# Kernel tuning notes

Hardware: AMD Instinct MI355X
Metric: run time of the kernel (lower is better)

Reference implementation:

```python
import jax, jax.numpy as jnp
import numpy as np

B, C, H, W = 8, 1024, 56, 56
NBINS = 256          # torch.histc(bins=256, min=0, max=1)
T_THRESH = 0.9       # EKLM entropy-ratio threshold
NUM_CLASSES = 30


def setup_inputs() -> dict:
    key = jax.random.key(0)
    k1, k2 = jax.random.split(key)
    x = jax.random.uniform(k1, (B, C, H, W), dtype=jnp.float32)
    w_fc = jax.random.normal(k2, (C, NUM_CLASSES), dtype=jnp.float32) * 0.02
    return {"x": x, "w_fc": w_fc}


def _integral_hist(x):
    """One fused pass replacing the per-region torch.histc calls.
    Returns per-(h,w)-cell histograms [H,W,256] and their 2D inclusive
    prefix sum padded to [H+1,W+1,256] so any rectangle histogram is 4 lookups.
    Matches torch.histc semantics: values outside [0,1] ignored, v==1 -> last bin."""
    valid = (x >= 0.0) & (x <= 1.0)
    q = jnp.clip(jnp.floor(x * NBINS), 0, NBINS - 1).astype(jnp.int32)
    q = jnp.where(valid, q, NBINS)  # out-of-range -> extra bin, dropped below
    hh = jnp.broadcast_to(jnp.arange(H)[None, None, :, None], x.shape)
    ww = jnp.broadcast_to(jnp.arange(W)[None, None, None, :], x.shape)
    cell = jnp.zeros((H, W, NBINS + 1), jnp.float32).at[hh, ww, q].add(1.0)[..., :NBINS]
    integ = jnp.cumsum(jnp.cumsum(cell, axis=0), axis=1)
    integ = jnp.pad(integ, ((1, 0), (1, 0), (0, 0)))  # [H+1, W+1, 256]
    return cell, integ


def _entropy_of_hist(h):
    p = h / jnp.sum(h)
    return -jnp.sum(p * jnp.log2(p + 1e-9))


def _region_entropy(integ, xs, xd, ys, yd):
    # histogram of x[:, :, xs:xd, ys:yd] via integral-histogram lookups
    h = integ[xd, yd] - integ[xs, yd] - integ[xd, ys] + integ[xs, ys]
    return _entropy_of_hist(h)


def eklm(x):
    """Entropy-based Key Localization Method (xs fixed to 0, as in source)."""
    cell, integ = _integral_hist(x)
    # compute_entropy_for_each_y: entropy of each [:, :, 0:1, y:y+1] column cell
    col_hists = cell[0]  # [W, 256]
    p = col_hists / jnp.sum(col_hists, axis=1, keepdims=True)
    ent_y = -jnp.sum(p * jnp.log2(p + 1e-9), axis=1)
    ys0 = jnp.argmax(ent_y).astype(jnp.int32)
    total_ent = _region_entropy(integ, 0, H, 0, W)

    def ent(xd, ys, yd):
        return _region_entropy(integ, 0, xd, ys, yd)

    def cond(state):
        xd, ys, yd, Ts, done = state
        return (Ts < T_THRESH) & (~done)

    def body(state):
        xd, ys, yd, Ts, done = state
        e_cur = ent(xd, ys, yd)
        # greedy priority identical to source: grow xd, else shrink ys, else grow yd
        c1 = (xd + 1 < H) & (ent(xd + 1, ys, yd) > e_cur)
        c2 = (~c1) & (ys - 1 >= 0) & (ent(xd, jnp.maximum(ys - 1, 0), yd) > e_cur)
        c3 = (~c1) & (~c2) & (yd + 1 < W) & (ent(xd, ys, jnp.minimum(yd + 1, W)) > e_cur)
        xd_n = jnp.where(c1, xd + 1, xd)
        ys_n = jnp.where(c2, ys - 1, ys)
        yd_n = jnp.where(c3, yd + 1, yd)
        done_n = ~(c1 | c2 | c3)
        Ts_n = ent(xd_n, ys_n, yd_n) / total_ent
        return (xd_n, ys_n, yd_n, Ts_n, done_n)

    xd0 = jnp.int32(1)
    yd0 = ys0 + jnp.int32(1)
    Ts0 = ent(xd0, ys0, yd0) / total_ent
    xd, ys, yd, _, _ = jax.lax.while_loop(
        cond, body, (xd0, ys0, yd0, Ts0, jnp.bool_(False)))
    return jnp.int32(0), xd, ys, yd


def reference(x, w_fc):
    xs, xd, ys, yd = eklm(x)
    # crop the located key region (mask form for static shapes), mean-pool, classify
    row = jnp.arange(H)
    col = jnp.arange(W)
    mask = ((row[:, None] >= xs) & (row[:, None] < xd)
            & (col[None, :] >= ys) & (col[None, :] < yd)).astype(x.dtype)
    area = jnp.maximum(jnp.sum(mask), 1.0)
    pooled = jnp.einsum('bchw,hw->bc', x, mask) / area  # [B, C]
    return pooled @ w_fc  # [B, NUM_CLASSES]
```

## Files before the change

### kernel.cpp

```cpp
#include <hip/hip_runtime.h>
#include <math.h>

#define BB 8
#define CC 1024
#define HH 56
#define WW 56
#define NB 256
#define NCLS 30
#define BC (BB * CC)
#define PLANE (HH * WW)
#define CELLS (HH * WW)
#define SLICES 16
#define WSPLIT 2
#define WHALF (WW / WSPLIT)
#define PL_PER_SLICE (BC / SLICES)
#define HTHREADS 256
#define VEC4_PER_BLOCK (PL_PER_SLICE * WHALF / 4)
#define HIST_ITERS (VEC4_PER_BLOCK / HTHREADS)

template <int PACK, bool ATOMIC_FLUSH>
__global__ __launch_bounds__(HTHREADS) void hist_kernel(const float* __restrict__ x,
                                                        unsigned* __restrict__ dst) {
    constexpr int WPW = NB / PACK;
    constexpr int PITCH = WPW + 1;
    constexpr int LH_TOT = WHALF * PITCH;
    constexpr int FLUSH_N = WPW * WHALF;
    __shared__ unsigned lh[LH_TOT];

    const int tid = threadIdx.x;
    const int g = blockIdx.x;
    const int whalf = (g >> 3) & 1;
    const int hs = ((g >> 4) << 3) | (g & 7);
    const int h = hs % HH;
    const int slice = hs / HH;

    for (int i = tid; i < LH_TOT; i += HTHREADS) lh[i] = 0u;
    __syncthreads();

    const float* __restrict__ xb =
        x + (size_t)(slice * PL_PER_SLICE) * PLANE + h * WW + whalf * WHALF;

#pragma unroll
    for (int it = 0; it < HIST_ITERS; ++it) {
        const int j = it * HTHREADS + tid;
        const int bcl = j / 7;
        const int wq = j - bcl * 7;
        const float4 v = *(const float4*)(xb + (size_t)bcl * PLANE + wq * 4);
        const float vv[4] = {v.x, v.y, v.z, v.w};
#pragma unroll
        for (int e = 0; e < 4; ++e) {
            const float f = vv[e];
            if (f >= 0.f && f <= 1.f) {
                int bin = (int)(f * 256.f);
                if (bin > 255) bin = 255;
                const int sh = (PACK == 4) ? ((bin & 3) << 3) : ((bin & 1) << 4);
                const int word = (PACK == 4) ? (bin >> 2) : (bin >> 1);
                atomicAdd(&lh[(wq * 4 + e) * PITCH + word], 1u << sh);
            }
        }
    }
    __syncthreads();

    for (int i = tid; i < FLUSH_N; i += HTHREADS) {
        const int word = i / WHALF;
        const int wl = i - word * WHALF;
        const unsigned v = lh[wl * PITCH + word];
        const int cell = h * WW + whalf * WHALF + wl;
        if (ATOMIC_FLUSH) {
            if (v) atomicAdd(&dst[(size_t)word * CELLS + cell], v);
        } else {
            dst[((size_t)word * SLICES + slice) * CELLS + cell] = v;
        }
    }
}

#define CPITCH 57
__global__ __launch_bounds__(256) void cum2d4_kernel(const unsigned* __restrict__ ps,
                                                     unsigned* __restrict__ integ) {
    __shared__ unsigned acc[4][HH * CPITCH];
    const int word = blockIdx.x;
    const unsigned* __restrict__ base = ps + (size_t)word * SLICES * CELLS;

    for (int c = threadIdx.x; c < CELLS; c += 256) {
        unsigned s0 = 0, s1 = 0, s2 = 0, s3 = 0;
#pragma unroll
        for (int sl = 0; sl < SLICES; ++sl) {
            const unsigned v = base[(size_t)sl * CELLS + c];
            s0 += v & 0xffu;
            s1 += (v >> 8) & 0xffu;
            s2 += (v >> 16) & 0xffu;
            s3 += v >> 24;
        }
        const int r = c / WW, w = c - r * WW;
        const int a_idx = r * CPITCH + w;
        acc[0][a_idx] = s0; acc[1][a_idx] = s1;
        acc[2][a_idx] = s2; acc[3][a_idx] = s3;
    }
    __syncthreads();

    if (threadIdx.x < 224) {
        const int a = threadIdx.x / HH, r = threadIdx.x % HH;
        unsigned run = 0;
        const int rb = r * CPITCH;
        for (int w = 0; w < WW; ++w) { run += acc[a][rb + w]; acc[a][rb + w] = run; }
    }
    __syncthreads();
    if (threadIdx.x < 224) {
        const int a = threadIdx.x / WW, cw = threadIdx.x % WW;
        unsigned run = 0;
        for (int hh = 0; hh < HH; ++hh) {
            run += acc[a][hh * CPITCH + cw];
            acc[a][hh * CPITCH + cw] = run;
        }
    }
    __syncthreads();

    for (int i = threadIdx.x; i < 4 * CELLS; i += 256) {
        const int a = i / CELLS, c = i - a * CELLS;
        const int r = c / WW, w = c - r * WW;
        integ[(size_t)(word * 4 + a) * CELLS + c] = acc[a][r * CPITCH + w];
    }
}

__global__ __launch_bounds__(256) void cum2d2_kernel(const unsigned* __restrict__ hp,
                                                     unsigned* __restrict__ integ) {
    __shared__ unsigned acc[CELLS];
    const int bin = blockIdx.x;
    const int word = bin >> 1;
    const int sh = (bin & 1) << 4;
    const unsigned* __restrict__ base = hp + (size_t)word * CELLS;

    for (int c = threadIdx.x; c < CELLS; c += 256)
        acc[c] = (base[c] >> sh) & 0xffffu;
    __syncthreads();
    if (threadIdx.x < HH) {
        unsigned run = 0;
        const int rb = threadIdx.x * WW;
        for (int w = 0; w < WW; ++w) { run += acc[rb + w]; acc[rb + w] = run; }
    }
    __syncthreads();
    if (threadIdx.x < WW) {
        unsigned run = 0;
        for (int hh = 0; hh < HH; ++hh) {
            run += acc[hh * WW + threadIdx.x];
            acc[hh * WW + threadIdx.x] = run;
        }
    }
    __syncthreads();
    unsigned* __restrict__ ob = integ + (size_t)bin * CELLS;
    for (int c = threadIdx.x; c < CELLS; c += 256) ob[c] = acc[c];
}

__device__ __forceinline__ float wave_sum(float v) {
#pragma unroll
    for (int off = 32; off > 0; off >>= 1) v += __shfl_xor(v, off);
    return v;
}

__device__ __forceinline__ float ilook(const unsigned* __restrict__ integ,
                                       int a, int b, int bin) {
    return (a == 0 || b == 0)
               ? 0.f
               : (float)integ[(size_t)bin * CELLS + (a - 1) * WW + (b - 1)];
}

__device__ float region_ent(const unsigned* __restrict__ integ, int lane,
                            int xd, int ys, int yd) {
    float hb[4];
    float hs = 0.f;
#pragma unroll
    for (int k = 0; k < 4; k++) {
        const int bin = lane + 64 * k;
        const float hv = ilook(integ, xd, yd, bin) - ilook(integ, xd, ys, bin);
        hb[k] = hv;
        hs += hv;
    }
    hs = wave_sum(hs);
    float e = 0.f;
#pragma unroll
    for (int k = 0; k < 4; k++) {
        const float p = hb[k] / hs;
        e += p * log2f(p + 1e-9f);
    }
    return -wave_sum(e);
}

__global__ __launch_bounds__(1024) void decide_kernel(const unsigned* __restrict__ integ,
                                                      int* __restrict__ region) {
    __shared__ float ent_s[WW];
    const int tid = threadIdx.x;
    const int lane = tid & 63;
    const int wv = tid >> 6;

    for (int w = wv; w < WW; w += 16) {
        float hb[4], hs = 0.f;
#pragma unroll
        for (int k = 0; k < 4; k++) {
            const int bin = lane + 64 * k;
            const float a = (float)integ[(size_t)bin * CELLS + w];
            const float b = w ? (float)integ[(size_t)bin * CELLS + w - 1] : 0.f;
            hb[k] = a - b;
            hs += hb[k];
        }
        hs = wave_sum(hs);
        float e = 0.f;
#pragma unroll
        for (int k = 0; k < 4; k++) {
            const float p = hb[k] / hs;
            e += p * log2f(p + 1e-9f);
        }
        e = -wave_sum(e);
        if (lane == 0) ent_s[w] = e;
    }
    __syncthreads();
    if (wv != 0) return;

    float best = -3.0e38f;
    int bestw = 0;
    for (int w = 0; w < WW; ++w) {
        const float e = ent_s[w];
        if (e > best) { best = e; bestw = w; }
    }

    const float total_ent = region_ent(integ, lane, HH, 0, WW);

    int xd = 1, ys = bestw, yd = bestw + 1;
    float Ts = region_ent(integ, lane, xd, ys, yd) / total_ent;
    bool done = false;
    int iter = 0;
    while (Ts < 0.9f && !done && iter < 1000) {
        iter++;
        const float e_cur = region_ent(integ, lane, xd, ys, yd);
        const int ysm = (ys - 1 < 0) ? 0 : ys - 1;
        const int ydp = (yd + 1 > WW) ? WW : yd + 1;
        const bool c1 = (xd + 1 < HH) && (region_ent(integ, lane, xd + 1, ys, yd) > e_cur);
        const bool c2 = !c1 && (ys - 1 >= 0) && (region_ent(integ, lane, xd, ysm, yd) > e_cur);
        const bool c3 = !c1 && !c2 && (yd + 1 < WW) && (region_ent(integ, lane, xd, ys, ydp) > e_cur);
        if (c1) xd = xd + 1;
        else if (c2) ys = ys - 1;
        else if (c3) yd = yd + 1;
        done = !(c1 || c2 || c3);
        Ts = region_ent(integ, lane, xd, ys, yd) / total_ent;
    }

    if (lane == 0) {
        region[0] = xd;
        region[1] = ys;
        region[2] = yd;
    }
}

__global__ void pool_kernel(const float* __restrict__ x,
                            const int* __restrict__ region,
                            float* __restrict__ pooled) {
    const int bc = blockIdx.x;
    const int xd = region[0], ys = region[1], yd = region[2];
    const int Wd = yd - ys;
    const int n = xd * Wd;
    const float area = fmaxf((float)n, 1.f);
    const float* plane = x + (size_t)bc * PLANE;
    float s = 0.f;
    for (int j = threadIdx.x; j < n; j += 64) {
        const int r = j / Wd;
        const int cc = ys + (j - r * Wd);
        s += plane[r * WW + cc];
    }
#pragma unroll
    for (int off = 32; off > 0; off >>= 1) s += __shfl_xor(s, off);
    if (threadIdx.x == 0) pooled[bc] = s / area;
}

__global__ __launch_bounds__(256) void fc_kernel(const float* __restrict__ pooled,
                                                 const float* __restrict__ wfc,
                                                 float* __restrict__ out) {
    __shared__ float red[240];
    const int b = blockIdx.x;
    const int t = threadIdx.x;
    if (t < 240) {
        const int chunk = t / NCLS;
        const int n = t - chunk * NCLS;
        const float* pv = pooled + b * CC + chunk * 128;
        const float* wv = wfc + (size_t)(chunk * 128) * NCLS + n;
        float a0 = 0.f, a1 = 0.f, a2 = 0.f, a3 = 0.f;
        for (int c = 0; c < 128; c += 4) {
            a0 += pv[c + 0] * wv[(c + 0) * NCLS];
            a1 += pv[c + 1] * wv[(c + 1) * NCLS];
            a2 += pv[c + 2] * wv[(c + 2) * NCLS];
            a3 += pv[c + 3] * wv[(c + 3) * NCLS];
        }
        red[t] = (a0 + a1) + (a2 + a3);
    }
    __syncthreads();
    if (t < NCLS) {
        float s = 0.f;
#pragma unroll
        for (int ch = 0; ch < 8; ++ch) s += red[ch * NCLS + t];
        out[b * NCLS + t] = s;
    }
}

extern "C" void kernel_launch(void* const* d_in, const int* in_sizes, int n_in,
                              void* d_out, int out_size, void* d_ws, size_t ws_size,
                              hipStream_t stream) {
    const float* x = (const float*)d_in[0];
    const float* wfc = (const float*)d_in[1];
    float* out = (float*)d_out;

    unsigned char* ws = (unsigned char*)d_ws;
    const size_t ps_bytes = (size_t)(NB / 4) * SLICES * CELLS * 4;
    const size_t integ_bytes = (size_t)NB * CELLS * 4;
    const size_t needA = ps_bytes + integ_bytes + 4096 + (size_t)BC * 4;

    if (ws_size >= needA) {
        unsigned* ps = (unsigned*)ws;
        unsigned* integ = (unsigned*)(ws + ps_bytes);
        int* region = (int*)(ws + ps_bytes + integ_bytes);
        float* pooled = (float*)(ws + ps_bytes + integ_bytes + 4096);

        hist_kernel<4, false><<<HH * WSPLIT * SLICES, HTHREADS, 0, stream>>>(x, ps);
        cum2d4_kernel<<<NB / 4, 256, 0, stream>>>(ps, integ);
        decide_kernel<<<1, 1024, 0, stream>>>(integ, region);
        pool_kernel<<<BC, 64, 0, stream>>>(x, region, pooled);
        fc_kernel<<<BB, 256, 0, stream>>>(pooled, wfc, out);
    } else {
        unsigned* hp = (unsigned*)ws;
        const size_t hp_bytes = (size_t)(NB / 2) * CELLS * 4;
        unsigned* integ = (unsigned*)(ws + hp_bytes);
        int* region = (int*)(ws + hp_bytes + integ_bytes);
        float* pooled = (float*)(ws + hp_bytes + integ_bytes + 4096);

        hipMemsetAsync(hp, 0, hp_bytes, stream);
        hist_kernel<2, true><<<HH * WSPLIT * SLICES, HTHREADS, 0, stream>>>(x, hp);
        cum2d2_kernel<<<NB, 256, 0, stream>>>(hp, integ);
        decide_kernel<<<1, 1024, 0, stream>>>(integ, region);
        pool_kernel<<<BC, 64, 0, stream>>>(x, region, pooled);
        fc_kernel<<<BB, 256, 0, stream>>>(pooled, wfc, out);
    }
}
```

Baseline: 194.9 us.

## Fuse cumsum with decide and pool with fc via last-block tickets

Cuts the pipeline from five kernels to three. The 2D prefix-sum kernel and the single-block decide kernel are merged: the last block to finish, detected with an atomic ticket, runs the decision. Pooling and the FC layer are merged the same way, with the last pool block computing all outputs. The histogram kernel resets the tickets, changes its block-to-cell mapping, and the pool blocks grow from 64 to 256 threads. The aim is to remove launch gaps, at the cost of serial tail work on one block and atomics plus fences in every block.

```diff
diff --git a/kernel.cpp b/kernel.cpp
--- a/kernel.cpp
+++ b/kernel.cpp
@@ -17,10 +17,13 @@
 #define HTHREADS 256
 #define VEC4_PER_BLOCK (PL_PER_SLICE * WHALF / 4)
 #define HIST_ITERS (VEC4_PER_BLOCK / HTHREADS)
+#define HGRID (HH * WSPLIT * SLICES)
+#define CPITCH 57
 
 template <int PACK, bool ATOMIC_FLUSH>
 __global__ __launch_bounds__(HTHREADS) void hist_kernel(const float* __restrict__ x,
-                                                        unsigned* __restrict__ dst) {
+                                                        unsigned* __restrict__ dst,
+                                                        unsigned* __restrict__ tickets) {
     constexpr int WPW = NB / PACK;
     constexpr int PITCH = WPW + 1;
     constexpr int LH_TOT = WHALF * PITCH;
@@ -28,9 +31,11 @@
     __shared__ unsigned lh[LH_TOT];
 
     const int tid = threadIdx.x;
-    const int g = blockIdx.x;
-    const int whalf = (g >> 3) & 1;
-    const int hs = ((g >> 4) << 3) | (g & 7);
+    const int bid = blockIdx.x;
+    if (bid == 0 && tid < 2) tickets[tid] = 0u;
+
+    const int whalf = bid & (WSPLIT - 1);
+    const int hs = bid / WSPLIT;
     const int h = hs % HH;
     const int slice = hs / HH;
 
@@ -74,83 +79,6 @@
     }
 }
 
-#define CPITCH 57
-__global__ __launch_bounds__(256) void cum2d4_kernel(const unsigned* __restrict__ ps,
-                                                     unsigned* __restrict__ integ) {
-    __shared__ unsigned acc[4][HH * CPITCH];
-    const int word = blockIdx.x;
-    const unsigned* __restrict__ base = ps + (size_t)word * SLICES * CELLS;
-
-    for (int c = threadIdx.x; c < CELLS; c += 256) {
-        unsigned s0 = 0, s1 = 0, s2 = 0, s3 = 0;
-#pragma unroll
-        for (int sl = 0; sl < SLICES; ++sl) {
-            const unsigned v = base[(size_t)sl * CELLS + c];
-            s0 += v & 0xffu;
-            s1 += (v >> 8) & 0xffu;
-            s2 += (v >> 16) & 0xffu;
-            s3 += v >> 24;
-        }
-        const int r = c / WW, w = c - r * WW;
-        const int a_idx = r * CPITCH + w;
-        acc[0][a_idx] = s0; acc[1][a_idx] = s1;
-        acc[2][a_idx] = s2; acc[3][a_idx] = s3;
-    }
-    __syncthreads();
-
-    if (threadIdx.x < 224) {
-        const int a = threadIdx.x / HH, r = threadIdx.x % HH;
-        unsigned run = 0;
-        const int rb = r * CPITCH;
-        for (int w = 0; w < WW; ++w) { run += acc[a][rb + w]; acc[a][rb + w] = run; }
-    }
-    __syncthreads();
-    if (threadIdx.x < 224) {
-        const int a = threadIdx.x / WW, cw = threadIdx.x % WW;
-        unsigned run = 0;
-        for (int hh = 0; hh < HH; ++hh) {
-            run += acc[a][hh * CPITCH + cw];
-            acc[a][hh * CPITCH + cw] = run;
-        }
-    }
-    __syncthreads();
-
-    for (int i = threadIdx.x; i < 4 * CELLS; i += 256) {
-        const int a = i / CELLS, c = i - a * CELLS;
-        const int r = c / WW, w = c - r * WW;
-        integ[(size_t)(word * 4 + a) * CELLS + c] = acc[a][r * CPITCH + w];
-    }
-}
-
-__global__ __launch_bounds__(256) void cum2d2_kernel(const unsigned* __restrict__ hp,
-                                                     unsigned* __restrict__ integ) {
-    __shared__ unsigned acc[CELLS];
-    const int bin = blockIdx.x;
-    const int word = bin >> 1;
-    const int sh = (bin & 1) << 4;
-    const unsigned* __restrict__ base = hp + (size_t)word * CELLS;
-
-    for (int c = threadIdx.x; c < CELLS; c += 256)
-        acc[c] = (base[c] >> sh) & 0xffffu;
-    __syncthreads();
-    if (threadIdx.x < HH) {
-        unsigned run = 0;
-        const int rb = threadIdx.x * WW;
-        for (int w = 0; w < WW; ++w) { run += acc[rb + w]; acc[rb + w] = run; }
-    }
-    __syncthreads();
-    if (threadIdx.x < WW) {
-        unsigned run = 0;
-        for (int hh = 0; hh < HH; ++hh) {
-            run += acc[hh * WW + threadIdx.x];
-            acc[hh * WW + threadIdx.x] = run;
-        }
-    }
-    __syncthreads();
-    unsigned* __restrict__ ob = integ + (size_t)bin * CELLS;
-    for (int c = threadIdx.x; c < CELLS; c += 256) ob[c] = acc[c];
-}
-
 __device__ __forceinline__ float wave_sum(float v) {
 #pragma unroll
     for (int off = 32; off > 0; off >>= 1) v += __shfl_xor(v, off);
@@ -185,14 +113,14 @@
     return -wave_sum(e);
 }
 
-__global__ __launch_bounds__(1024) void decide_kernel(const unsigned* __restrict__ integ,
-                                                      int* __restrict__ region) {
-    __shared__ float ent_s[WW];
+__device__ void decide_body(const unsigned* __restrict__ integ,
+                            int* __restrict__ region, float* ent_s) {
     const int tid = threadIdx.x;
     const int lane = tid & 63;
     const int wv = tid >> 6;
-
-    for (int w = wv; w < WW; w += 16) {
+    const int nw = blockDim.x >> 6;
+
+    for (int w = wv; w < WW; w += nw) {
         float hb[4], hs = 0.f;
 #pragma unroll
         for (int k = 0; k < 4; k++) {
@@ -250,52 +178,157 @@
     }
 }
 
-__global__ void pool_kernel(const float* __restrict__ x,
-                            const int* __restrict__ region,
-                            float* __restrict__ pooled) {
+__global__ __launch_bounds__(1024) void cum2d4_decide_kernel(
+    const unsigned* __restrict__ ps, unsigned* __restrict__ integ,
+    int* __restrict__ region, unsigned* __restrict__ tickets) {
+    __shared__ unsigned acc[4][HH * CPITCH];
+    __shared__ float ent_s[WW];
+    __shared__ unsigned ticket;
+    const int word = blockIdx.x;
+    const unsigned* __restrict__ base = ps + (size_t)word * SLICES * CELLS;
+
+    for (int c = threadIdx.x; c < CELLS; c += 1024) {
+        unsigned s0 = 0, s1 = 0, s2 = 0, s3 = 0;
+#pragma unroll
+        for (int sl = 0; sl < SLICES; ++sl) {
+            const unsigned v = base[(size_t)sl * CELLS + c];
+            s0 += v & 0xffu;
+            s1 += (v >> 8) & 0xffu;
+            s2 += (v >> 16) & 0xffu;
+            s3 += v >> 24;
+        }
+        const int r = c / WW, w = c - r * WW;
+        const int ai = r * CPITCH + w;
+        acc[0][ai] = s0; acc[1][ai] = s1; acc[2][ai] = s2; acc[3][ai] = s3;
+    }
+    __syncthreads();
+
+    if (threadIdx.x < 224) {
+        const int a = threadIdx.x / HH, r = threadIdx.x % HH;
+        unsigned run = 0;
+        const int rb = r * CPITCH;
+        for (int w = 0; w < WW; ++w) { run += acc[a][rb + w]; acc[a][rb + w] = run; }
+    }
+    __syncthreads();
+    if (threadIdx.x < 224) {
+        const int a = threadIdx.x / WW, cw = threadIdx.x % WW;
+        unsigned run = 0;
+        for (int hh = 0; hh < HH; ++hh) {
+            run += acc[a][hh * CPITCH + cw];
+            acc[a][hh * CPITCH + cw] = run;
+        }
+    }
+    __syncthreads();
+
+    for (int i = threadIdx.x; i < 4 * CELLS; i += 1024) {
+        const int a = i / CELLS, c = i - a * CELLS;
+        const int r = c / WW, w = c - r * WW;
+        integ[(size_t)(word * 4 + a) * CELLS + c] = acc[a][r * CPITCH + w];
+    }
+
+    __syncthreads();
+    __threadfence();
+    if (threadIdx.x == 0) ticket = atomicAdd(&tickets[0], 1u);
+    __syncthreads();
+    if (ticket == 63) {
+        __threadfence();
+        decide_body(integ, region, ent_s);
+    }
+}
+
+__global__ __launch_bounds__(256) void cum2d2_decide_kernel(
+    const unsigned* __restrict__ hp, unsigned* __restrict__ integ,
+    int* __restrict__ region, unsigned* __restrict__ tickets) {
+    __shared__ unsigned acc[HH * CPITCH];
+    __shared__ float ent_s[WW];
+    __shared__ unsigned ticket;
+    const int bin = blockIdx.x;
+    const int word = bin >> 1;
+    const int sh = (bin & 1) << 4;
+    const unsigned* __restrict__ base = hp + (size_t)word * CELLS;
+
+    for (int c = threadIdx.x; c < CELLS; c += 256) {
+        const int r = c / WW, w = c - r * WW;
+        acc[r * CPITCH + w] = (base[c] >> sh) & 0xffffu;
+    }
+    __syncthreads();
+    if (threadIdx.x < HH) {
+        unsigned run = 0;
+        const int rb = threadIdx.x * CPITCH;
+        for (int w = 0; w < WW; ++w) { run += acc[rb + w]; acc[rb + w] = run; }
+    }
+    __syncthreads();
+    if (threadIdx.x < WW) {
+        unsigned run = 0;
+        for (int hh = 0; hh < HH; ++hh) {
+            run += acc[hh * CPITCH + threadIdx.x];
+            acc[hh * CPITCH + threadIdx.x] = run;
+        }
+    }
+    __syncthreads();
+    for (int c = threadIdx.x; c < CELLS; c += 256) {
+        const int r = c / WW, w = c - r * WW;
+        integ[(size_t)bin * CELLS + c] = acc[r * CPITCH + w];
+    }
+
+    __syncthreads();
+    __threadfence();
+    if (threadIdx.x == 0) ticket = atomicAdd(&tickets[0], 1u);
+    __syncthreads();
+    if (ticket == 255) {
+        __threadfence();
+        decide_body(integ, region, ent_s);
+    }
+}
+
+__global__ __launch_bounds__(256) void pool_fc_kernel(
+    const float* __restrict__ x, const int* __restrict__ region,
+    float* __restrict__ pooled, const float* __restrict__ wfc,
+    float* __restrict__ out, unsigned* __restrict__ tickets) {
+    __shared__ float wpart[4];
+    __shared__ unsigned ticket;
+    const int tid = threadIdx.x;
+    const int lane = tid & 63;
+    const int wv = tid >> 6;
     const int bc = blockIdx.x;
     const int xd = region[0], ys = region[1], yd = region[2];
     const int Wd = yd - ys;
     const int n = xd * Wd;
     const float area = fmaxf((float)n, 1.f);
     const float* plane = x + (size_t)bc * PLANE;
+
     float s = 0.f;
-    for (int j = threadIdx.x; j < n; j += 64) {
+    for (int j = tid; j < n; j += 256) {
         const int r = j / Wd;
         const int cc = ys + (j - r * Wd);
         s += plane[r * WW + cc];
     }
 #pragma unroll
     for (int off = 32; off > 0; off >>= 1) s += __shfl_xor(s, off);
-    if (threadIdx.x == 0) pooled[bc] = s / area;
-}
-
-__global__ __launch_bounds__(256) void fc_kernel(const float* __restrict__ pooled,
-                                                 const float* __restrict__ wfc,
-                                                 float* __restrict__ out) {
-    __shared__ float red[240];
-    const int b = blockIdx.x;
-    const int t = threadIdx.x;
-    if (t < 240) {
-        const int chunk = t / NCLS;
-        const int n = t - chunk * NCLS;
-        const float* pv = pooled + b * CC + chunk * 128;
-        const float* wv = wfc + (size_t)(chunk * 128) * NCLS + n;
-        float a0 = 0.f, a1 = 0.f, a2 = 0.f, a3 = 0.f;
-        for (int c = 0; c < 128; c += 4) {
-            a0 += pv[c + 0] * wv[(c + 0) * NCLS];
-            a1 += pv[c + 1] * wv[(c + 1) * NCLS];
-            a2 += pv[c + 2] * wv[(c + 2) * NCLS];
-            a3 += pv[c + 3] * wv[(c + 3) * NCLS];
-        }
-        red[t] = (a0 + a1) + (a2 + a3);
-    }
-    __syncthreads();
-    if (t < NCLS) {
-        float s = 0.f;
-#pragma unroll
-        for (int ch = 0; ch < 8; ++ch) s += red[ch * NCLS + t];
-        out[b * NCLS + t] = s;
+    if (lane == 0) wpart[wv] = s;
+    __syncthreads();
+
+    if (tid == 0) {
+        pooled[bc] = (wpart[0] + wpart[1] + wpart[2] + wpart[3]) / area;
+        __threadfence();
+        ticket = atomicAdd(&tickets[1], 1u);
+    }
+    __syncthreads();
+
+    if (ticket == BC - 1) {
+        __threadfence();
+        for (int o = tid; o < BB * NCLS; o += 256) {
+            const int b = o / NCLS, cls = o - b * NCLS;
+            const float* pv = pooled + b * CC;
+            float a0 = 0.f, a1 = 0.f, a2 = 0.f, a3 = 0.f;
+            for (int c = 0; c < CC; c += 4) {
+                a0 += pv[c + 0] * wfc[(c + 0) * NCLS + cls];
+                a1 += pv[c + 1] * wfc[(c + 1) * NCLS + cls];
+                a2 += pv[c + 2] * wfc[(c + 2) * NCLS + cls];
+                a3 += pv[c + 3] * wfc[(c + 3) * NCLS + cls];
+            }
+            out[o] = (a0 + a1) + (a2 + a3);
+        }
     }
 }
 
@@ -314,26 +347,26 @@
     if (ws_size >= needA) {
         unsigned* ps = (unsigned*)ws;
         unsigned* integ = (unsigned*)(ws + ps_bytes);
-        int* region = (int*)(ws + ps_bytes + integ_bytes);
-        float* pooled = (float*)(ws + ps_bytes + integ_bytes + 4096);
-
-        hist_kernel<4, false><<<HH * WSPLIT * SLICES, HTHREADS, 0, stream>>>(x, ps);
-        cum2d4_kernel<<<NB / 4, 256, 0, stream>>>(ps, integ);
-        decide_kernel<<<1, 1024, 0, stream>>>(integ, region);
-        pool_kernel<<<BC, 64, 0, stream>>>(x, region, pooled);
-        fc_kernel<<<BB, 256, 0, stream>>>(pooled, wfc, out);
+        unsigned char* tail = ws + ps_bytes + integ_bytes;
+        int* region = (int*)tail;
+        unsigned* tickets = (unsigned*)(tail + 64);
+        float* pooled = (float*)(tail + 4096);
+
+        hist_kernel<4, false><<<HGRID, HTHREADS, 0, stream>>>(x, ps, tickets);
+        cum2d4_decide_kernel<<<NB / 4, 1024, 0, stream>>>(ps, integ, region, tickets);
+        pool_fc_kernel<<<BC, 256, 0, stream>>>(x, region, pooled, wfc, out, tickets);
     } else {
         unsigned* hp = (unsigned*)ws;
         const size_t hp_bytes = (size_t)(NB / 2) * CELLS * 4;
         unsigned* integ = (unsigned*)(ws + hp_bytes);
-        int* region = (int*)(ws + hp_bytes + integ_bytes);
-        float* pooled = (float*)(ws + hp_bytes + integ_bytes + 4096);
+        unsigned char* tail = ws + hp_bytes + integ_bytes;
+        int* region = (int*)tail;
+        unsigned* tickets = (unsigned*)(tail + 64);
+        float* pooled = (float*)(tail + 4096);
 
         hipMemsetAsync(hp, 0, hp_bytes, stream);
-        hist_kernel<2, true><<<HH * WSPLIT * SLICES, HTHREADS, 0, stream>>>(x, hp);
-        cum2d2_kernel<<<NB, 256, 0, stream>>>(hp, integ);
-        decide_kernel<<<1, 1024, 0, stream>>>(integ, region);
-        pool_kernel<<<BC, 64, 0, stream>>>(x, region, pooled);
-        fc_kernel<<<BB, 256, 0, stream>>>(pooled, wfc, out);
-    }
-}
+        hist_kernel<2, true><<<HGRID, HTHREADS, 0, stream>>>(x, hp, tickets);
+        cum2d2_decide_kernel<<<NB, 256, 0, stream>>>(hp, integ, region, tickets);
+        pool_fc_kernel<<<BC, 256, 0, stream>>>(x, region, pooled, wfc, out, tickets);
+    }
+}
```

New measurement: 390.1 us. +100.2%, slower.
